# Performance work log

Hardware: AMD Instinct MI355X
Metric: run time of the kernel (lower is better)

## Reference

```python
import jax, jax.numpy as jnp
import numpy as np

N_EMBD = 1024
HEAD_SIZE = 128


def setup_inputs() -> dict:
    key = jax.random.key(0)
    k_x, k_w, k_cov, k_b = jax.random.split(key, 4)
    x = jax.random.normal(k_x, (16384, 2, N_EMBD), dtype=jnp.float32)
    # values_proj: nn.Linear(n_embd, head_size, bias=False) -> weight [head_size, n_embd]
    W = jax.random.normal(k_w, (HEAD_SIZE, N_EMBD), dtype=jnp.float32) * (N_EMBD ** -0.5)
    cov = jax.random.normal(k_cov, (HEAD_SIZE, HEAD_SIZE), dtype=jnp.float32) * (HEAD_SIZE ** -0.5)
    bias = jax.random.normal(k_b, (HEAD_SIZE,), dtype=jnp.float32)
    return {"x": x, "W": W, "cov": cov, "bias": bias}


def reference(x, W, cov, bias):
    # x: [B, 2, E]; W: [H, E]; cov: [H, H]; bias: [H]
    values = jnp.einsum('be,he->bh', x[:, 0, :], W)  # [B, H]
    mask = jnp.einsum('be,he->bh', x[:, 1, :], W)    # [B, H]
    # diag_embed(mask) @ cov == mask[:, :, None] * cov  -> [B, H, H]
    coeffs = jax.nn.softmax(mask[:, :, None] * cov[None, :, :], axis=-1)
    # values.unsqueeze(1) @ coeffs + bias, then [:, 0, :]
    out = jnp.einsum('bh,bhk->bk', values, coeffs) + bias
    return out
```

## Files before the change

### kernel.cpp

```cpp
#include <hip/hip_runtime.h>

#define LOG2E 1.4426950408889634f

typedef __attribute__((ext_vector_type(8))) short frag_ab;
typedef __attribute__((ext_vector_type(4))) float frag_cd;

__device__ inline short f2bf(float f) {
    union { float f; unsigned u; } v; v.f = f;
    unsigned r = v.u + 0x7fffu + ((v.u >> 16) & 1u);
    return (short)(r >> 16);
}

template<int CTRL>
__device__ inline float dpp_ror_add(float x) {
    int t = __builtin_amdgcn_update_dpp(0, __builtin_bit_cast(int, x), CTRL, 0xf, 0xf, false);
    return x + __builtin_bit_cast(float, t);
}

#define PACK_AF(af, p0, p1)                                                   \
    af[0] = f2bf(p0.x); af[1] = f2bf(p0.y); af[2] = f2bf(p0.z); af[3] = f2bf(p0.w); \
    af[4] = f2bf(p1.x); af[5] = f2bf(p1.y); af[6] = f2bf(p1.z); af[7] = f2bf(p1.w);

__global__ __launch_bounds__(256) void prep_kernel(const float* __restrict__ W,
                                                   short* __restrict__ wbf) {
    int g = blockIdx.x * 256 + threadIdx.x;
    int h = g >> 7;
    int k0 = (g & 127) << 3;
    const float* src = W + h * 1024 + k0;
    float4 w0 = *(const float4*)src;
    float4 w1 = *(const float4*)(src + 4);
    frag_ab af;
    PACK_AF(af, w0, w1);
    int c = k0 >> 6, s = (k0 >> 5) & 1, kg = (k0 >> 3) & 3;
    int nt = h >> 4, m = h & 15, lane = kg * 16 + m;
    int dst = (((c * 8 + nt) * 2 + s) * 64 + lane) * 8;
    *(frag_ab*)(wbf + dst) = af;
}

__global__ __launch_bounds__(256, 4) void proj_kernel(const float* __restrict__ x,
                                                      const short* __restrict__ wbf,
                                                      float* __restrict__ vm) {
    const int tid = threadIdx.x;
    const int lane = tid & 63, wave = tid >> 6;
    const int rg = wave & 1, nh = wave >> 1;
    const int m = lane & 15, kg = lane >> 4;
    const long rowbase = (long)blockIdx.x * 32 + rg * 16;
    const float* xrow = x + (rowbase + m) * 1024 + kg * 8;
    const frag_ab* wb = (const frag_ab*)wbf + lane;

    frag_cd acc[4];
#pragma unroll
    for (int ntl = 0; ntl < 4; ++ntl) acc[ntl] = (frag_cd){0.f, 0.f, 0.f, 0.f};

    float4 a0 = *(const float4*)(xrow);
    float4 a1 = *(const float4*)(xrow + 4);
    float4 a2 = *(const float4*)(xrow + 32);
    float4 a3 = *(const float4*)(xrow + 36);

    for (int c = 0; c < 16; ++c) {
        float4 n0, n1, n2, n3;
        if (c < 15) {
            const float* xn = xrow + (c + 1) * 64;
            n0 = *(const float4*)(xn);
            n1 = *(const float4*)(xn + 4);
            n2 = *(const float4*)(xn + 32);
            n3 = *(const float4*)(xn + 36);
        }
        frag_ab af0, af1;
        PACK_AF(af0, a0, a1);
        PACK_AF(af1, a2, a3);

        const frag_ab* bp = wb + ((size_t)c * 8 + nh * 4) * 2 * 64;
#pragma unroll
        for (int ntl = 0; ntl < 4; ++ntl) {
            frag_ab bf0 = bp[(ntl * 2 + 0) * 64];
            acc[ntl] = __builtin_amdgcn_mfma_f32_16x16x32_bf16(af0, bf0, acc[ntl], 0, 0, 0);
            frag_ab bf1 = bp[(ntl * 2 + 1) * 64];
            acc[ntl] = __builtin_amdgcn_mfma_f32_16x16x32_bf16(af1, bf1, acc[ntl], 0, 0, 0);
        }
        if (c < 15) { a0 = n0; a1 = n1; a2 = n2; a3 = n3; }
    }

#pragma unroll
    for (int ntl = 0; ntl < 4; ++ntl)
#pragma unroll
        for (int r = 0; r < 4; ++r) {
            long row = rowbase + kg * 4 + r;
            vm[row * 128 + (nh * 4 + ntl) * 16 + m] = acc[ntl][r];
        }
}

__global__ __launch_bounds__(512, 4) void combine_kernel(const float* __restrict__ vm,
                                                         const float* __restrict__ cov,
                                                         const float* __restrict__ bias,
                                                         float* __restrict__ out) {
    __shared__ float obuf[4][32][132];

    const int t = threadIdx.x;
    const int i = t >> 4;
    const int j = t & 15;
    const float bias_own = bias[t & 127];

    float covreg[4][8];
#pragma unroll
    for (int hh = 0; hh < 4; ++hh) {
        const float* cr = cov + (long)(i * 4 + hh) * 128 + j * 8;
        float4 c0 = *(const float4*)cr;
        float4 c1 = *(const float4*)(cr + 4);
        covreg[hh][0] = LOG2E * c0.x; covreg[hh][1] = LOG2E * c0.y;
        covreg[hh][2] = LOG2E * c0.z; covreg[hh][3] = LOG2E * c0.w;
        covreg[hh][4] = LOG2E * c1.x; covreg[hh][5] = LOG2E * c1.y;
        covreg[hh][6] = LOG2E * c1.z; covreg[hh][7] = LOG2E * c1.w;
    }

    const long b0 = (long)blockIdx.x * 8;
    for (int rr = 0; rr < 2; ++rr) {
#pragma unroll
        for (int sb = 0; sb < 4; ++sb) {
            const long b = b0 + rr * 4 + sb;
            float4 v4 = *(const float4*)(vm + (2 * b) * 128 + i * 4);
            float4 m4 = *(const float4*)(vm + (2 * b + 1) * 128 + i * 4);
            float vh[4] = {v4.x, v4.y, v4.z, v4.w};
            float mh[4] = {m4.x, m4.y, m4.z, m4.w};
            float op[8] = {0.f, 0.f, 0.f, 0.f, 0.f, 0.f, 0.f, 0.f};
#pragma unroll
            for (int hh = 0; hh < 4; ++hh) {
                float mv = mh[hh];
                float p[8];
#pragma unroll
                for (int kk = 0; kk < 8; ++kk)
                    p[kk] = __builtin_amdgcn_exp2f(mv * covreg[hh][kk]);
                float s0 = p[0] + p[1], s1 = p[2] + p[3];
                float s2 = p[4] + p[5], s3 = p[6] + p[7];
                float lsum = (s0 + s1) + (s2 + s3);
                lsum = dpp_ror_add<0x121>(lsum);
                lsum = dpp_ror_add<0x122>(lsum);
                lsum = dpp_ror_add<0x124>(lsum);
                lsum = dpp_ror_add<0x128>(lsum);
                float w = vh[hh] * __builtin_amdgcn_rcpf(lsum);
#pragma unroll
                for (int kk = 0; kk < 8; ++kk) op[kk] = fmaf(w, p[kk], op[kk]);
            }
            *(float4*)&obuf[sb][i][j * 8]     = make_float4(op[0], op[1], op[2], op[3]);
            *(float4*)&obuf[sb][i][j * 8 + 4] = make_float4(op[4], op[5], op[6], op[7]);
        }
        __syncthreads();
        {
            const int k  = t & 127;
            const int sb = t >> 7;
            float o = bias_own;
#pragma unroll
            for (int ii = 0; ii < 32; ++ii) o += obuf[sb][ii][k];
            out[(b0 + rr * 4 + sb) * 128 + k] = o;
        }
        __syncthreads();
    }
}

extern "C" void kernel_launch(void* const* d_in, const int* in_sizes, int n_in,
                              void* d_out, int out_size, void* d_ws, size_t ws_size,
                              hipStream_t stream) {
    const float* x    = (const float*)d_in[0];
    const float* W    = (const float*)d_in[1];
    const float* cov  = (const float*)d_in[2];
    const float* bias = (const float*)d_in[3];
    float* out = (float*)d_out;

    const int B = in_sizes[0] / (2 * 1024);

    short* wbf = (short*)d_ws;
    float* vm  = (float*)(wbf + 128 * 1024);

    prep_kernel<<<64, 256, 0, stream>>>(W, wbf);
    proj_kernel<<<(2 * B) / 32, 256, 0, stream>>>(x, wbf, vm);
    combine_kernel<<<B / 8, 512, 0, stream>>>(vm, cov, bias, out);
}
```

Measured before the change: 267.0 us.

## Deepen x prefetch to two chunks in proj and shrink combine LDS buffer

Measured after the change: 276.8 us. 1.04x slower.

```diff
diff --git a/kernel.cpp b/kernel.cpp
--- a/kernel.cpp
+++ b/kernel.cpp
@@ -52,33 +52,57 @@
 #pragma unroll
     for (int ntl = 0; ntl < 4; ++ntl) acc[ntl] = (frag_cd){0.f, 0.f, 0.f, 0.f};
 
-    float4 a0 = *(const float4*)(xrow);
-    float4 a1 = *(const float4*)(xrow + 4);
-    float4 a2 = *(const float4*)(xrow + 32);
-    float4 a3 = *(const float4*)(xrow + 36);
-
-    for (int c = 0; c < 16; ++c) {
-        float4 n0, n1, n2, n3;
-        if (c < 15) {
-            const float* xn = xrow + (c + 1) * 64;
-            n0 = *(const float4*)(xn);
-            n1 = *(const float4*)(xn + 4);
-            n2 = *(const float4*)(xn + 32);
-            n3 = *(const float4*)(xn + 36);
-        }
-        frag_ab af0, af1;
-        PACK_AF(af0, a0, a1);
-        PACK_AF(af1, a2, a3);
-
-        const frag_ab* bp = wb + ((size_t)c * 8 + nh * 4) * 2 * 64;
-#pragma unroll
-        for (int ntl = 0; ntl < 4; ++ntl) {
-            frag_ab bf0 = bp[(ntl * 2 + 0) * 64];
-            acc[ntl] = __builtin_amdgcn_mfma_f32_16x16x32_bf16(af0, bf0, acc[ntl], 0, 0, 0);
-            frag_ab bf1 = bp[(ntl * 2 + 1) * 64];
-            acc[ntl] = __builtin_amdgcn_mfma_f32_16x16x32_bf16(af1, bf1, acc[ntl], 0, 0, 0);
-        }
-        if (c < 15) { a0 = n0; a1 = n1; a2 = n2; a3 = n3; }
+    float4 aA0 = *(const float4*)(xrow);
+    float4 aA1 = *(const float4*)(xrow + 4);
+    float4 aA2 = *(const float4*)(xrow + 32);
+    float4 aA3 = *(const float4*)(xrow + 36);
+    float4 aB0 = *(const float4*)(xrow + 64);
+    float4 aB1 = *(const float4*)(xrow + 68);
+    float4 aB2 = *(const float4*)(xrow + 96);
+    float4 aB3 = *(const float4*)(xrow + 100);
+
+    for (int cc = 0; cc < 8; ++cc) {
+        const int c0 = 2 * cc, c1 = 2 * cc + 1;
+        {
+            frag_ab af0, af1;
+            PACK_AF(af0, aA0, aA1);
+            PACK_AF(af1, aA2, aA3);
+            if (c0 + 2 < 16) {
+                const float* xn = xrow + (c0 + 2) * 64;
+                aA0 = *(const float4*)(xn);
+                aA1 = *(const float4*)(xn + 4);
+                aA2 = *(const float4*)(xn + 32);
+                aA3 = *(const float4*)(xn + 36);
+            }
+            const frag_ab* bp = wb + ((size_t)c0 * 8 + nh * 4) * 2 * 64;
+#pragma unroll
+            for (int ntl = 0; ntl < 4; ++ntl) {
+                frag_ab bf0 = bp[(ntl * 2 + 0) * 64];
+                acc[ntl] = __builtin_amdgcn_mfma_f32_16x16x32_bf16(af0, bf0, acc[ntl], 0, 0, 0);
+                frag_ab bf1 = bp[(ntl * 2 + 1) * 64];
+                acc[ntl] = __builtin_amdgcn_mfma_f32_16x16x32_bf16(af1, bf1, acc[ntl], 0, 0, 0);
+            }
+        }
+        {
+            frag_ab af0, af1;
+            PACK_AF(af0, aB0, aB1);
+            PACK_AF(af1, aB2, aB3);
+            if (c1 + 2 < 16) {
+                const float* xn = xrow + (c1 + 2) * 64;
+                aB0 = *(const float4*)(xn);
+                aB1 = *(const float4*)(xn + 4);
+                aB2 = *(const float4*)(xn + 32);
+                aB3 = *(const float4*)(xn + 36);
+            }
+            const frag_ab* bp = wb + ((size_t)c1 * 8 + nh * 4) * 2 * 64;
+#pragma unroll
+            for (int ntl = 0; ntl < 4; ++ntl) {
+                frag_ab bf0 = bp[(ntl * 2 + 0) * 64];
+                acc[ntl] = __builtin_amdgcn_mfma_f32_16x16x32_bf16(af0, bf0, acc[ntl], 0, 0, 0);
+                frag_ab bf1 = bp[(ntl * 2 + 1) * 64];
+                acc[ntl] = __builtin_amdgcn_mfma_f32_16x16x32_bf16(af1, bf1, acc[ntl], 0, 0, 0);
+            }
+        }
     }
 
 #pragma unroll
@@ -94,7 +118,7 @@
                                                          const float* __restrict__ cov,
                                                          const float* __restrict__ bias,
                                                          float* __restrict__ out) {
-    __shared__ float obuf[4][32][132];
+    __shared__ float obuf[2][32][132];
 
     const int t = threadIdx.x;
     const int i = t >> 4;
@@ -114,10 +138,10 @@
     }
 
     const long b0 = (long)blockIdx.x * 8;
-    for (int rr = 0; rr < 2; ++rr) {
-#pragma unroll
-        for (int sb = 0; sb < 4; ++sb) {
-            const long b = b0 + rr * 4 + sb;
+    for (int rr = 0; rr < 4; ++rr) {
+#pragma unroll
+        for (int sb = 0; sb < 2; ++sb) {
+            const long b = b0 + rr * 2 + sb;
             float4 v4 = *(const float4*)(vm + (2 * b) * 128 + i * 4);
             float4 m4 = *(const float4*)(vm + (2 * b + 1) * 128 + i * 4);
             float vh[4] = {v4.x, v4.y, v4.z, v4.w};
@@ -145,13 +169,13 @@
             *(float4*)&obuf[sb][i][j * 8 + 4] = make_float4(op[4], op[5], op[6], op[7]);
         }
         __syncthreads();
-        {
+        if (t < 256) {
             const int k  = t & 127;
             const int sb = t >> 7;
             float o = bias_own;
 #pragma unroll
             for (int ii = 0; ii < 32; ++ii) o += obuf[sb][ii][k];
-            out[(b0 + rr * 4 + sb) * 128 + k] = o;
+            out[(b0 + rr * 2 + sb) * 128 + k] = o;
         }
         __syncthreads();
     }
```
